# Kernel optimization log

Measured on AMD Instinct MI355X. Metric: run time of the kernel, lower is better.

## Reference

```python
import jax, jax.numpy as jnp
import numpy as np

# DeepSeek-style MLA decode paged attention (vLLM HPU flat_pa_mla, latent cache path)
B = 32              # batch (decode requests)
H = 16              # q heads (TP shard)
KV_LORA = 512       # kv_lora_rank
ROPE = 64           # qk_rope_head_dim
D = KV_LORA + ROPE  # 576, latent+rope dim
BS = 128            # block_size
BLOCKS_PER_SEQ = 16 # 2048-token context
NB = B * BLOCKS_PER_SEQ   # 512 active blocks
NCACHE = 1024       # blocks in the paged cache
SCALE = 192 ** -0.5  # 1/sqrt(qk_nope(128)+rope(64))
NEG = -1.0e9


def setup_inputs() -> dict:
    key = jax.random.key(0)
    k1, k2, k3, k4 = jax.random.split(key, 4)
    query = jax.random.normal(k1, (B, H, D), dtype=jnp.float32)
    key_cache = jax.random.normal(k2, (NCACHE, BS, D), dtype=jnp.float32)
    # each active block points at some cache block
    block_list = jax.random.randint(k3, (NB,), 0, NCACHE, dtype=jnp.int32)
    # contiguous grouping: blocks_per_seq blocks per request
    block_groups = jnp.repeat(jnp.arange(B, dtype=jnp.int32), BLOCKS_PER_SEQ)
    block_mapping = jax.nn.one_hot(block_groups, B, dtype=jnp.float32)  # [NB, B]
    # per-block usage in [1, BS]; unused tail positions masked out
    usage = jax.random.randint(k4, (NB,), 1, BS + 1)
    block_bias = jnp.where(jnp.arange(BS)[None, :] < usage[:, None], 0.0, NEG).astype(jnp.float32)
    return {"query": query, "key_cache": key_cache, "block_mapping": block_mapping,
            "block_bias": block_bias, "block_list": block_list, "block_groups": block_groups}


def reference(query, key_cache, block_mapping, block_bias, block_list, block_groups):
    # batch2block: scatter per-batch query to its blocks via one-hot matmul
    q = SCALE * jnp.einsum('nb,bhd->nhd', block_mapping, query)      # [NB,H,D]
    kv = key_cache[block_list]                                       # [NB,BS,D] fetched latent KV
    v = kv[..., :KV_LORA]                                            # [NB,BS,V]
    attn = jnp.einsum('nhd,nsd->nhs', q, kv) + block_bias[:, None, :]  # [NB,H,BS]
    # per-block online softmax pieces
    block_max = attn.max(axis=-1, keepdims=True)                     # [NB,H,1]
    p = jnp.exp(attn - block_max)
    block_sums = p.sum(axis=-1)                                      # [NB,H]
    o = jnp.einsum('nhs,nsv->nhv', p, v)                             # [NB,H,V]
    bm = block_max[..., 0]                                           # [NB,H]
    # grouped max over blocks of the same request, broadcast back to blocks
    group_max = jax.ops.segment_max(bm, block_groups, num_segments=B)[block_groups]
    adj = jnp.exp(bm - group_max)                                    # [NB,H]
    sum_adj = block_sums * adj
    # block2batch then batch2block of the adjusted sums
    group_sum = jnp.einsum('nb,nh->bh', block_mapping, sum_adj)
    group_sum = jnp.einsum('nb,bh->nh', block_mapping, group_sum)
    group_sum = jnp.maximum(group_sum, sum_adj)
    rescale = adj / group_sum
    o = o * rescale[..., None]
    # block2batch: sum rescaled partial outputs per request
    out = jnp.einsum('nb,nhv->bhv', block_mapping, o)                # [B,H,V]
    return out
```

## Files before the change

### kernel.cpp

```cpp
#include <hip/hip_runtime.h>
#include <math.h>

#define NB_ 512
#define B_ 32
#define H_ 16
#define D_ 576
#define KV_ 512
#define BS_ 128
#define STR 580
#define SCALE_ 0.07216878364870323f

__device__ float g_o[NB_ * H_ * KV_];
__device__ float g_bm[NB_ * H_];
__device__ float g_bs[NB_ * H_];

__global__ __launch_bounds__(256) void mla_block_kernel(
    const float* __restrict__ query,
    const float* __restrict__ key_cache,
    const float* __restrict__ block_bias,
    const int* __restrict__ block_list,
    const int* __restrict__ block_groups)
{
    __shared__ float q_s[H_ * STR];
    __shared__ float kt[16 * STR];
    __shared__ float p_s[H_ * 16];
    __shared__ float alpha_s[H_];

    const int tid = threadIdx.x;
    const int n   = blockIdx.x;
    const int b   = block_groups[n];
    const float* K = key_cache + (long)block_list[n] * (BS_ * D_);
    const float* Q = query + (long)b * (H_ * D_);

#pragma unroll
    for (int i = 0; i < 9; ++i) {
        int flat = tid + 256 * i;
        int row = flat / 144;
        int c4  = flat - row * 144;
        float4 v = *(const float4*)(Q + row * D_ + 4 * c4);
        v.x *= SCALE_; v.y *= SCALE_; v.z *= SCALE_; v.w *= SCALE_;
        *(float4*)(q_s + row * STR + 4 * c4) = v;
    }

    const int hg  = tid >> 6;
    const int sl  = tid & 63;
    const int h2  = sl >> 4;
    const int s16 = sl & 15;
    const int h   = 4 * hg + h2;

    float m_run = -1e30f;
    float l_run = 0.f;
    float4 oa0[4], oa1[4];
#pragma unroll
    for (int i = 0; i < 4; ++i) {
        oa0[i] = make_float4(0.f, 0.f, 0.f, 0.f);
        oa1[i] = make_float4(0.f, 0.f, 0.f, 0.f);
    }

    for (int sc = 0; sc < BS_; sc += 16) {
        __syncthreads();
#pragma unroll
        for (int i = 0; i < 9; ++i) {
            int flat = tid + 256 * i;
            int row = flat / 144;
            int c4  = flat - row * 144;
            *(float4*)(kt + row * STR + 4 * c4) =
                *(const float4*)(K + (long)(sc + row) * D_ + 4 * c4);
        }
        __syncthreads();

        float acc = 0.f;
#pragma unroll 4
        for (int d = 0; d < D_; d += 4) {
            float4 kv = *(const float4*)(kt + s16 * STR + d);
            float4 qv = *(const float4*)(q_s + h * STR + d);
            acc += qv.x * kv.x + qv.y * kv.y + qv.z * kv.z + qv.w * kv.w;
        }
        float logit = acc + block_bias[n * BS_ + sc + s16];

        float mc = logit;
#pragma unroll
        for (int off = 1; off < 16; off <<= 1) mc = fmaxf(mc, __shfl_xor(mc, off));
        float m_new = fmaxf(m_run, mc);
        float alpha = __expf(m_run - m_new);
        float p = __expf(logit - m_new);
        float psum = p;
#pragma unroll
        for (int off = 1; off < 16; off <<= 1) psum += __shfl_xor(psum, off);
        l_run = l_run * alpha + psum;
        m_run = m_new;
        p_s[h * 16 + s16] = p;
        if (s16 == 0) alpha_s[h] = alpha;
        __syncthreads();

        float a[4];
#pragma unroll
        for (int i = 0; i < 4; ++i) a[i] = alpha_s[4 * hg + i];
#pragma unroll
        for (int i = 0; i < 4; ++i) {
            oa0[i].x *= a[i]; oa0[i].y *= a[i]; oa0[i].z *= a[i]; oa0[i].w *= a[i];
            oa1[i].x *= a[i]; oa1[i].y *= a[i]; oa1[i].z *= a[i]; oa1[i].w *= a[i];
        }
#pragma unroll 4
        for (int s = 0; s < 16; ++s) {
            float4 v0 = *(const float4*)(kt + s * STR + 4 * sl);
            float4 v1 = *(const float4*)(kt + s * STR + 256 + 4 * sl);
#pragma unroll
            for (int i = 0; i < 4; ++i) {
                float pv = p_s[(4 * hg + i) * 16 + s];
                oa0[i].x += pv * v0.x; oa0[i].y += pv * v0.y;
                oa0[i].z += pv * v0.z; oa0[i].w += pv * v0.w;
                oa1[i].x += pv * v1.x; oa1[i].y += pv * v1.y;
                oa1[i].z += pv * v1.z; oa1[i].w += pv * v1.w;
            }
        }
    }

    if (s16 == 0) {
        g_bm[n * H_ + h] = m_run;
        g_bs[n * H_ + h] = l_run;
    }
    float* op = g_o + (long)n * H_ * KV_;
#pragma unroll
    for (int i = 0; i < 4; ++i) {
        *(float4*)(op + (4 * hg + i) * KV_ + 4 * sl) = oa0[i];
        *(float4*)(op + (4 * hg + i) * KV_ + 256 + 4 * sl) = oa1[i];
    }
}

__global__ __launch_bounds__(128) void mla_combine_kernel(float* __restrict__ out)
{
    const int bh = blockIdx.x;
    const int b = bh >> 4;
    const int h = bh & 15;
    const int tid = threadIdx.x;

    float bm[16];
    float m = -1e30f;
#pragma unroll
    for (int j = 0; j < 16; ++j) {
        bm[j] = g_bm[(16 * b + j) * H_ + h];
        m = fmaxf(m, bm[j]);
    }
    float sa[16];
    float gs = 0.f;
#pragma unroll
    for (int j = 0; j < 16; ++j) {
        sa[j] = g_bs[(16 * b + j) * H_ + h] * __expf(bm[j] - m);
        gs += sa[j];
    }
    float4 acc = make_float4(0.f, 0.f, 0.f, 0.f);
#pragma unroll
    for (int j = 0; j < 16; ++j) {
        float r = __expf(bm[j] - m) / fmaxf(gs, sa[j]);
        const float4 v = *(const float4*)(g_o + ((long)((16 * b + j) * H_ + h)) * KV_ + 4 * tid);
        acc.x += r * v.x; acc.y += r * v.y;
        acc.z += r * v.z; acc.w += r * v.w;
    }
    *(float4*)(out + (long)bh * KV_ + 4 * tid) = acc;
}

extern "C" void kernel_launch(void* const* d_in, const int* in_sizes, int n_in,
                              void* d_out, int out_size, void* d_ws, size_t ws_size,
                              hipStream_t stream)
{
    const float* query        = (const float*)d_in[0];
    const float* key_cache    = (const float*)d_in[1];
    const float* block_bias   = (const float*)d_in[3];
    const int*   block_list   = (const int*)d_in[4];
    const int*   block_groups = (const int*)d_in[5];
    float* out = (float*)d_out;

    mla_block_kernel<<<NB_, 256, 0, stream>>>(query, key_cache, block_bias,
                                              block_list, block_groups);
    mla_combine_kernel<<<B_ * H_, 128, 0, stream>>>(out);
}
```

Baseline: 403.4 us.

## Register-tile QK dot products with split-d reduction and vectorize P loads

Replaces the per-thread full-length 576-wide dot product with a 4x4 head-by-token register micro-tile. The d dimension is split across 16 groups of 36, with partial sums reduced through shuffles and a small shared buffer. This cuts LDS reads per FMA in the score phase. It also prefetches the block bias into registers, reads P as float4 in the PV loop, and changes the shared row stride to 578, which no longer keeps rows 16-byte aligned for the float4 LDS accesses and so risks misaligned vector loads.

```diff
diff --git a/kernel.cpp b/kernel.cpp
--- a/kernel.cpp
+++ b/kernel.cpp
@@ -7,7 +7,7 @@
 #define D_ 576
 #define KV_ 512
 #define BS_ 128
-#define STR 580
+#define STR 578
 #define SCALE_ 0.07216878364870323f
 
 __device__ float g_o[NB_ * H_ * KV_];
@@ -23,6 +23,7 @@
 {
     __shared__ float q_s[H_ * STR];
     __shared__ float kt[16 * STR];
+    __shared__ float red[4 * 256];
     __shared__ float p_s[H_ * 16];
     __shared__ float alpha_s[H_];
 
@@ -48,6 +49,15 @@
     const int s16 = sl & 15;
     const int h   = 4 * hg + h2;
 
+    const int sq    = tid & 3;
+    const int hq    = (tid >> 2) & 3;
+    const int dgrp  = tid >> 4;
+    const int dbase = dgrp * 36;
+
+    float bias[8];
+#pragma unroll
+    for (int c = 0; c < 8; ++c) bias[c] = block_bias[n * BS_ + 16 * c + s16];
+
     float m_run = -1e30f;
     float l_run = 0.f;
     float4 oa0[4], oa1[4];
@@ -57,7 +67,7 @@
         oa1[i] = make_float4(0.f, 0.f, 0.f, 0.f);
     }
 
-    for (int sc = 0; sc < BS_; sc += 16) {
+    for (int sc8 = 0; sc8 < 8; ++sc8) {
         __syncthreads();
 #pragma unroll
         for (int i = 0; i < 9; ++i) {
@@ -65,19 +75,56 @@
             int row = flat / 144;
             int c4  = flat - row * 144;
             *(float4*)(kt + row * STR + 4 * c4) =
-                *(const float4*)(K + (long)(sc + row) * D_ + 4 * c4);
-        }
-        __syncthreads();
-
-        float acc = 0.f;
-#pragma unroll 4
-        for (int d = 0; d < D_; d += 4) {
-            float4 kv = *(const float4*)(kt + s16 * STR + d);
-            float4 qv = *(const float4*)(q_s + h * STR + d);
-            acc += qv.x * kv.x + qv.y * kv.y + qv.z * kv.z + qv.w * kv.w;
-        }
-        float logit = acc + block_bias[n * BS_ + sc + s16];
-
+                *(const float4*)(K + (long)(sc8 * 16 + row) * D_ + 4 * c4);
+        }
+        __syncthreads();
+
+        float c[4][4];
+#pragma unroll
+        for (int i = 0; i < 4; ++i)
+#pragma unroll
+            for (int jj = 0; jj < 4; ++jj) c[i][jj] = 0.f;
+
+#pragma unroll
+        for (int j = 0; j < 9; ++j) {
+            float4 qv[4], kv[4];
+#pragma unroll
+            for (int i = 0; i < 4; ++i)
+                qv[i] = *(const float4*)(q_s + (4 * hq + i) * STR + dbase + 4 * j);
+#pragma unroll
+            for (int i = 0; i < 4; ++i)
+                kv[i] = *(const float4*)(kt + (4 * sq + i) * STR + dbase + 4 * j);
+#pragma unroll
+            for (int i = 0; i < 4; ++i)
+#pragma unroll
+                for (int jj = 0; jj < 4; ++jj)
+                    c[i][jj] += qv[i].x * kv[jj].x + qv[i].y * kv[jj].y +
+                                qv[i].z * kv[jj].z + qv[i].w * kv[jj].w;
+        }
+#pragma unroll
+        for (int i = 0; i < 4; ++i)
+#pragma unroll
+            for (int jj = 0; jj < 4; ++jj) {
+                float v = c[i][jj];
+                v += __shfl_xor(v, 16);
+                v += __shfl_xor(v, 32);
+                c[i][jj] = v;
+            }
+        if (sl < 16) {
+#pragma unroll
+            for (int i = 0; i < 4; ++i)
+#pragma unroll
+                for (int jj = 0; jj < 4; ++jj)
+                    red[hg * 256 + sl * 16 + i * 4 + jj] = c[i][jj];
+        }
+        __syncthreads();
+
+        float logit = bias[sc8];
+        {
+            const int rbase = (4 * hg + (s16 >> 2)) * 16 + h2 * 4 + (s16 & 3);
+#pragma unroll
+            for (int w = 0; w < 4; ++w) logit += red[w * 256 + rbase];
+        }
         float mc = logit;
 #pragma unroll
         for (int off = 1; off < 16; off <<= 1) mc = fmaxf(mc, __shfl_xor(mc, off));
@@ -101,17 +148,26 @@
             oa0[i].x *= a[i]; oa0[i].y *= a[i]; oa0[i].z *= a[i]; oa0[i].w *= a[i];
             oa1[i].x *= a[i]; oa1[i].y *= a[i]; oa1[i].z *= a[i]; oa1[i].w *= a[i];
         }
-#pragma unroll 4
-        for (int s = 0; s < 16; ++s) {
-            float4 v0 = *(const float4*)(kt + s * STR + 4 * sl);
-            float4 v1 = *(const float4*)(kt + s * STR + 256 + 4 * sl);
-#pragma unroll
-            for (int i = 0; i < 4; ++i) {
-                float pv = p_s[(4 * hg + i) * 16 + s];
-                oa0[i].x += pv * v0.x; oa0[i].y += pv * v0.y;
-                oa0[i].z += pv * v0.z; oa0[i].w += pv * v0.w;
-                oa1[i].x += pv * v1.x; oa1[i].y += pv * v1.y;
-                oa1[i].z += pv * v1.z; oa1[i].w += pv * v1.w;
+#pragma unroll
+        for (int s4 = 0; s4 < 4; ++s4) {
+            float4 pf[4];
+#pragma unroll
+            for (int i = 0; i < 4; ++i)
+                pf[i] = *(const float4*)(p_s + (4 * hg + i) * 16 + 4 * s4);
+#pragma unroll
+            for (int jj = 0; jj < 4; ++jj) {
+                int s = 4 * s4 + jj;
+                float4 v0 = *(const float4*)(kt + s * STR + 4 * sl);
+                float4 v1 = *(const float4*)(kt + s * STR + 256 + 4 * sl);
+#pragma unroll
+                for (int i = 0; i < 4; ++i) {
+                    const float* pfp = (const float*)&pf[i];
+                    float pv = pfp[jj];
+                    oa0[i].x += pv * v0.x; oa0[i].y += pv * v0.y;
+                    oa0[i].z += pv * v0.z; oa0[i].w += pv * v0.w;
+                    oa1[i].x += pv * v1.x; oa1[i].y += pv * v1.y;
+                    oa1[i].z += pv * v1.z; oa1[i].w += pv * v1.w;
+                }
             }
         }
     }
```

New measurement: 421.3 us. 4.4% more time.
